# Kernel tuning notes

Measured on AMD Instinct MI355X. Metric: run time of the kernel, lower is better.

Reference implementation:

```python
import jax, jax.numpy as jnp
import numpy as np

N = 50000       # population nodes
E = 1_600_000   # edges per edge type
F_IN = 2000     # flattened individual-graph embedding (100*20)
D = 20          # hidden channels per TransformerConv head (heads=1)
NEG_SLOPE = 0.01
BN_EPS = 1e-5


def setup_inputs() -> dict:
    key = jax.random.key(0)
    ks = jax.random.split(key, 24)
    features = jax.random.normal(ks[0], (N, F_IN), jnp.float32)
    same_index = jax.random.randint(ks[1], (2, E), 0, N, dtype=jnp.int64)
    diff_index = jax.random.randint(ks[2], (2, E), 0, N, dtype=jnp.int64)
    s0 = 1.0 / np.sqrt(F_IN)
    s1 = 1.0 / np.sqrt(D)
    # layer 0 conv params, stacked over the 2 edge types (same, diff)
    W0q = jax.random.normal(ks[3], (2, F_IN, D), jnp.float32) * s0
    W0k = jax.random.normal(ks[4], (2, F_IN, D), jnp.float32) * s0
    W0v = jax.random.normal(ks[5], (2, F_IN, D), jnp.float32) * s0
    W0s = jax.random.normal(ks[6], (2, F_IN, D), jnp.float32) * s0
    b0q = jnp.zeros((2, D)); b0k = jnp.zeros((2, D))
    b0v = jnp.zeros((2, D)); b0s = jnp.zeros((2, D))
    # layers 1..3 conv params: [layer, edge_type, D, D]
    Wq = jax.random.normal(ks[7], (3, 2, D, D), jnp.float32) * s1
    Wk = jax.random.normal(ks[8], (3, 2, D, D), jnp.float32) * s1
    Wv = jax.random.normal(ks[9], (3, 2, D, D), jnp.float32) * s1
    Ws = jax.random.normal(ks[10], (3, 2, D, D), jnp.float32) * s1
    bq = jnp.zeros((3, 2, D)); bk = jnp.zeros((3, 2, D))
    bv = jnp.zeros((3, 2, D)); bs = jnp.zeros((3, 2, D))
    w1 = jnp.full((4,), 0.8, jnp.float32)
    w2 = jnp.full((4,), 0.2, jnp.float32)
    bn_gamma = jnp.ones((4, D), jnp.float32)
    bn_beta = jnp.zeros((4, D), jnp.float32)
    Wout = jax.random.normal(ks[11], (4 * D, 2), jnp.float32) / np.sqrt(4 * D)
    bout = jnp.zeros((2,), jnp.float32)
    return dict(features=features, same_index=same_index, diff_index=diff_index,
                W0q=W0q, b0q=b0q, W0k=W0k, b0k=b0k, W0v=W0v, b0v=b0v, W0s=W0s, b0s=b0s,
                Wq=Wq, bq=bq, Wk=Wk, bk=bk, Wv=Wv, bv=bv, Ws=Ws, bs=bs,
                w1=w1, w2=w2, bn_gamma=bn_gamma, bn_beta=bn_beta, Wout=Wout, bout=bout)


def _tconv(x, edge_index, Wq, bq, Wk, bk, Wv, bv, Ws, bs):
    """PyG TransformerConv, heads=1, concat=True, root_weight=True, no edge_attr."""
    src, dst = edge_index[0], edge_index[1]
    q = x @ Wq + bq   # [N, D]
    k = x @ Wk + bk
    v = x @ Wv + bv
    logits = jnp.einsum('ed,ed->e', q[dst], k[src]) / jnp.sqrt(jnp.float32(D))  # [E]
    m = jax.ops.segment_max(logits, dst, num_segments=N)
    m = jnp.where(jnp.isfinite(m), m, jnp.float32(0.0))  # nodes with no in-edges
    e = jnp.exp(logits - m[dst])
    z = jax.ops.segment_sum(e, dst, num_segments=N)
    alpha = e / (z[dst] + 1e-16)  # PyG softmax epsilon
    agg = jax.ops.segment_sum(alpha[:, None] * v[src], dst, num_segments=N)  # [N, D]
    return agg + x @ Ws + bs  # skip (root) connection


def _bn(x, gamma, beta):
    mu = x.mean(axis=0)
    var = x.var(axis=0)
    return (x - mu) * jax.lax.rsqrt(var + BN_EPS) * gamma + beta


def reference(features, same_index, diff_index,
              W0q, b0q, W0k, b0k, W0v, b0v, W0s, b0s,
              Wq, bq, Wk, bk, Wv, bv, Ws, bs,
              w1, w2, bn_gamma, bn_beta, Wout, bout):
    x = features
    fcs = []
    for l in range(4):
        if l == 0:
            p_same = (W0q[0], b0q[0], W0k[0], b0k[0], W0v[0], b0v[0], W0s[0], b0s[0])
            p_diff = (W0q[1], b0q[1], W0k[1], b0k[1], W0v[1], b0v[1], W0s[1], b0s[1])
        else:
            i = l - 1
            p_same = (Wq[i, 0], bq[i, 0], Wk[i, 0], bk[i, 0], Wv[i, 0], bv[i, 0], Ws[i, 0], bs[i, 0])
            p_diff = (Wq[i, 1], bq[i, 1], Wk[i, 1], bk[i, 1], Wv[i, 1], bv[i, 1], Ws[i, 1], bs[i, 1])
        x1 = _tconv(x, same_index, *p_same)
        x2 = _tconv(x, diff_index, *p_diff)
        t = w1[l] + w2[l]
        x = (w1[l] / t) * x1 + (w2[l] / t) * x2
        x = _bn(x, bn_gamma[l], bn_beta[l])
        x = jax.nn.leaky_relu(x, NEG_SLOPE)
        fcs.append(x)
    fc = jnp.concatenate(fcs, axis=-1)  # [N, 80]
    return fc @ Wout + bout  # [N, 2]
```

## Files before the change

### kernel.cpp

```cpp
#include <hip/hip_runtime.h>
#include <math.h>

#define N_NODES 50000
#define E_EDGES 1600000
#define F_IN    2000
#define D       20
#define NCOL    160
#define KPAD    2016
#define NBNP    64

#define INV_SQRT_D 0.22360679774997896f

typedef __bf16 bf16x8 __attribute__((ext_vector_type(8)));
typedef __bf16 bf16x4 __attribute__((ext_vector_type(4)));
typedef float  f32x4  __attribute__((ext_vector_type(4)));


__global__ void pack_kernel(
    const float* __restrict__ W0q, const float* __restrict__ W0k,
    const float* __restrict__ W0v, const float* __restrict__ W0s,
    const float* __restrict__ b0q, const float* __restrict__ b0k,
    const float* __restrict__ b0v, const float* __restrict__ b0s,
    const float* __restrict__ Wq,  const float* __restrict__ Wk,
    const float* __restrict__ Wv,  const float* __restrict__ Ws_,
    const float* __restrict__ bq,  const float* __restrict__ bk,
    const float* __restrict__ bv,  const float* __restrict__ bs_,
    __bf16* __restrict__ B0, float* __restrict__ bias0,
    float* __restrict__ WL, float* __restrict__ biasL,
    float* __restrict__ bnp, int* __restrict__ deg)
{
  long idx = (long)blockIdx.x * blockDim.x + threadIdx.x;
  if (idx < (long)NCOL*KPAD) {
    int col = (int)(idx / KPAD), k = (int)(idx % KPAD);
    int et = col / 80, r = col % 80, mat = r / 20, d = r % 20;
    const float* w = (mat==0)?W0q:(mat==1)?W0s:(mat==2)?W0k:W0v;
    float v = (k < F_IN) ? w[((size_t)et*F_IN + k)*D + d] : 0.f;
    B0[idx] = (__bf16)v;
    return;
  }
  idx -= (long)NCOL*KPAD;
  if (idx < 160) {
    int col = (int)idx;
    int et = col / 80, r = col % 80, mat = r / 20, d = r % 20;
    const float* b = (mat==0)?b0q:(mat==1)?b0s:(mat==2)?b0k:b0v;
    bias0[col] = b[et*D + d];
    return;
  }
  idx -= 160;
  if (idx < 9600) {
    int l = (int)(idx / 3200), rem = (int)(idx % 3200);
    int k = rem / NCOL, col = rem % NCOL;
    int et = col / 80, r = col % 80, mat = r / 20, d = r % 20;
    const float* w = (mat==0)?Wq:(mat==1)?Ws_:(mat==2)?Wk:Wv;
    WL[idx] = w[(((size_t)l*2 + et)*D + k)*D + d];
    return;
  }
  idx -= 9600;
  if (idx < 480) {
    int l = (int)(idx / NCOL), col = (int)(idx % NCOL);
    int et = col / 80, r = col % 80, mat = r / 20, d = r % 20;
    const float* b = (mat==0)?bq:(mat==1)?bs_:(mat==2)?bk:bv;
    biasL[idx] = b[(l*2 + et)*D + d];
    return;
  }
  idx -= 480;
  if (idx < 4*NBNP*40) { bnp[idx] = 0.f; return; }
  idx -= 4*NBNP*40;
  if (idx < 2*N_NODES) { deg[idx] = 0; return; }
}

__global__ void hist_kernel(const int* __restrict__ same, const int* __restrict__ diff,
                            int* __restrict__ deg)
{
  long i = (long)blockIdx.x * blockDim.x + threadIdx.x;
  if (i >= 2L*E_EDGES) return;
  int et = (i >= E_EDGES) ? 1 : 0;
  long e = i - (long)et*E_EDGES;
  const int* ix = et ? diff : same;
  int dst = ix[E_EDGES + e];
  atomicAdd(&deg[(size_t)et*N_NODES + dst], 1);
}

__global__ void scan_kernel(const int* __restrict__ deg,
                            int* __restrict__ rowptr0, int* __restrict__ rowptr1,
                            int* __restrict__ next0, int* __restrict__ next1)
{
  const int et = blockIdx.x;
  const int* dg = deg + (size_t)et*N_NODES;
  int* rp = et ? rowptr1 : rowptr0;
  int* np = et ? next1 : next0;
  __shared__ int part[1024];
  const int t = threadIdx.x;
  const int per = (N_NODES + 1023) / 1024;
  const int b = t * per;
  const int e = (b + per < N_NODES) ? (b + per) : N_NODES;
  int s = 0;
  for (int i = b; i < e; i++) s += dg[i];
  part[t] = s;
  __syncthreads();
  for (int o = 1; o < 1024; o <<= 1) {
    int v = (t >= o) ? part[t-o] : 0;
    __syncthreads();
    part[t] += v;
    __syncthreads();
  }
  int run = (t == 0) ? 0 : part[t-1];
  for (int i = b; i < e; i++) {
    rp[i] = run; np[i] = run;
    run += dg[i];
  }
  if (t == 0) rp[N_NODES] = part[1023];
}

#define SC_EPT 16
#define SC_CHUNK (256*SC_EPT)
__global__ void scatter_kernel(const int* __restrict__ same, const int* __restrict__ diff,
                               int* __restrict__ next0, int* __restrict__ next1,
                               int* __restrict__ adj0, int* __restrict__ adj1)
{
  const int part  = blockIdx.x & 7;
  const int chunk = blockIdx.x >> 3;
  const int lo = part * (N_NODES/8);
  const int hi = lo + (N_NODES/8);
  const long i0 = (long)chunk * SC_CHUNK + threadIdx.x;
#pragma unroll
  for (int it = 0; it < SC_EPT; ++it) {
    long i = i0 + (long)it*256;
    if (i >= 2L*E_EDGES) break;
    int et = (i >= E_EDGES) ? 1 : 0;
    long e = i - (long)et*E_EDGES;
    const int* ix = et ? diff : same;
    int dst = ix[E_EDGES + e];
    if (dst >= lo && dst < hi) {
      int src = ix[e];
      int* np  = et ? next1 : next0;
      int* adj = et ? adj1  : adj0;
      int pos = atomicAdd(&np[dst], 1);
      adj[pos] = src;
    }
  }
}

__launch_bounds__(512)
__global__ void gemm0_mfma(const float* __restrict__ A,
                           const __bf16* __restrict__ Bt,
                           const float* __restrict__ bias,
                           __bf16* __restrict__ QS,
                           __bf16* __restrict__ KV0, __bf16* __restrict__ KV1)
{
  __shared__ __bf16 as[128*32];
  const int t    = threadIdx.x;
  const int lane = t & 63;
  const int wid  = t >> 6;
  const int wr   = wid >> 1;
  const int wc   = wid & 1;
  const int rb0  = blockIdx.x * 128;

  const int srow = t >> 2;
  const int skc  = (t & 3) * 8;
  const int arow = rb0 + srow;
  const float* aptr = A + (size_t)arow * F_IN;

  const int lrow = lane & 15;
  const int lkb  = (lane >> 4) * 8;

  f32x4 acc[2][5];
#pragma unroll
  for (int i = 0; i < 2; i++)
#pragma unroll
    for (int j = 0; j < 5; j++) acc[i][j] = (f32x4){0.f,0.f,0.f,0.f};

  float4 p0, p1;
  auto loadA = [&](int k0) {
    int k = k0 + skc;
    if (arow < N_NODES) {
      if (k + 8 <= F_IN) {
        p0 = *(const float4*)(aptr + k);
        p1 = *(const float4*)(aptr + k + 4);
      } else {
        float tmp[8];
#pragma unroll
        for (int i = 0; i < 8; i++) tmp[i] = (k + i < F_IN) ? aptr[k + i] : 0.f;
        p0 = make_float4(tmp[0],tmp[1],tmp[2],tmp[3]);
        p1 = make_float4(tmp[4],tmp[5],tmp[6],tmp[7]);
      }
    } else {
      p0 = make_float4(0,0,0,0); p1 = p0;
    }
  };

  loadA(0);
  for (int s = 0; s < 63; s++) {
    bf16x8 h;
    h[0]=(__bf16)p0.x; h[1]=(__bf16)p0.y; h[2]=(__bf16)p0.z; h[3]=(__bf16)p0.w;
    h[4]=(__bf16)p1.x; h[5]=(__bf16)p1.y; h[6]=(__bf16)p1.z; h[7]=(__bf16)p1.w;
    *(bf16x8*)&as[srow*32 + skc] = h;
    __syncthreads();
    if (s + 1 < 63) loadA((s + 1) * 32);

    bf16x8 af[2];
#pragma unroll
    for (int rf = 0; rf < 2; rf++)
      af[rf] = *(bf16x8*)&as[(wr*32 + rf*16 + lrow)*32 + lkb];
    bf16x8 bfr[5];
#pragma unroll
    for (int cf = 0; cf < 5; cf++)
      bfr[cf] = *(const bf16x8*)(Bt + (size_t)(wc*80 + cf*16 + lrow)*KPAD + s*32 + lkb);
#pragma unroll
    for (int rf = 0; rf < 2; rf++)
#pragma unroll
      for (int cf = 0; cf < 5; cf++)
        acc[rf][cf] = __builtin_amdgcn_mfma_f32_16x16x32_bf16(af[rf], bfr[cf], acc[rf][cf], 0, 0, 0);
    __syncthreads();
  }

#pragma unroll
  for (int rf = 0; rf < 2; rf++) {
#pragma unroll
    for (int cf = 0; cf < 5; cf++) {
      int col = wc*80 + cf*16 + lrow;
      int et = col / 80, r = col % 80, mat = r / 20, d = r % 20;
      float bv = bias[col];
      __bf16* kvp = et ? KV1 : KV0;
#pragma unroll
      for (int j = 0; j < 4; j++) {
        int row = rb0 + wr*32 + rf*16 + (lane >> 4)*4 + j;
        if (row < N_NODES) {
          __bf16 val = (__bf16)(acc[rf][cf][j] + bv);
          if (mat < 2) QS[(size_t)row*80 + et*40 + mat*20 + d] = val;
          else         kvp[(size_t)row*64 + (mat-2)*20 + d]   = val;
        }
      }
    }
  }
}

__launch_bounds__(256)
__global__ void proj_small_kernel(const float* __restrict__ xp, const float* __restrict__ bnl,
                                  const float* __restrict__ gam, const float* __restrict__ bet,
                                  const float* __restrict__ W, const float* __restrict__ bias,
                                  __bf16* __restrict__ QS,
                                  __bf16* __restrict__ KV0, __bf16* __restrict__ KV1)
{
  __shared__ float ws[20*160];
  __shared__ float xs[16*20];
  __shared__ float Ac[20], Bc[20];
  const int t = threadIdx.x;
  const int n0 = blockIdx.x * 16;
#pragma unroll
  for (int i = 0; i < 13; i++) {
    int idx = t + i*256;
    if (idx < 3200) ws[idx] = W[idx];
  }
  if (t < 20) {
    float s1 = 0.f, s2 = 0.f;
    for (int s = 0; s < NBNP; s++) { s1 += bnl[s*40 + t]; s2 += bnl[s*40 + 20 + t]; }
    float mu  = s1 * (1.f/N_NODES);
    float var = s2 * (1.f/N_NODES) - mu*mu;
    float a = rsqrtf(var + 1e-5f) * gam[t];
    Ac[t] = a; Bc[t] = bet[t] - mu*a;
  }
  __syncthreads();
#pragma unroll
  for (int i = 0; i < 2; i++) {
    int idx = t + i*256;
    if (idx < 320) {
      int nl = idx / 20, k = idx % 20;
      int n = n0 + nl;
      float x = (n < N_NODES) ? xp[(size_t)n*D + k] : 0.f;
      float y = x*Ac[k] + Bc[k];
      xs[idx] = (y > 0.f) ? y : 0.01f*y;
    }
  }
  __syncthreads();
#pragma unroll
  for (int i = 0; i < 10; i++) {
    int idx = t + i*256;
    int nl = idx / NCOL, col = idx % NCOL;
    int n = n0 + nl;
    if (n < N_NODES) {
      float acc = bias[col];
#pragma unroll
      for (int k = 0; k < 20; k++) acc += xs[nl*20 + k] * ws[k*NCOL + col];
      int et = col / 80, r = col % 80, mat = r / 20, d = r % 20;
      __bf16 val = (__bf16)acc;
      if (mat < 2) QS[(size_t)n*80 + et*40 + mat*20 + d] = val;
      else         (et ? KV1 : KV0)[(size_t)n*64 + (mat-2)*20 + d] = val;
    }
  }
}

__launch_bounds__(256)
__global__ void attn_fused(const int* __restrict__ rp0, const int* __restrict__ adj0,
                           const int* __restrict__ rp1, const int* __restrict__ adj1,
                           const __bf16* __restrict__ QS,
                           const __bf16* __restrict__ KV0, const __bf16* __restrict__ KV1,
                           const float* __restrict__ w1, const float* __restrict__ w2, int l,
                           float* __restrict__ xpre, float* __restrict__ bnp)
{
  __shared__ float xnode[4][20];
  const int t    = threadIdx.x;
  const int wv   = t >> 6;
  const int lane = t & 63;
  const int half = lane >> 5;
  const int sl   = lane & 31;
  const int node = blockIdx.x*4 + wv;

  const int* rowptr = half ? rp1 : rp0;
  const int* adj    = half ? adj1 : adj0;
  const __bf16* kvb = half ? KV1 : KV0;
  const __bf16* rq  = QS + (size_t)node*80 + half*40;

  float qf[20];
  {
    bf16x8 q0 = *(const bf16x8*)(rq);
    bf16x8 q1 = *(const bf16x8*)(rq + 8);
    bf16x4 q2 = *(const bf16x4*)(rq + 16);
#pragma unroll
    for (int i = 0; i < 8; i++) { qf[i] = (float)q0[i]; qf[8+i] = (float)q1[i]; }
#pragma unroll
    for (int i = 0; i < 4; i++) qf[16+i] = (float)q2[i];
  }

  const int beg = rowptr[node], end = rowptr[node+1];
  float z = 0.f;
  float S[20];
#pragma unroll
  for (int d = 0; d < 20; d++) S[d] = 0.f;

  for (int i = beg + sl; i < end; i += 32) {
    const int src = adj[i];
    const __bf16* kv = kvb + (size_t)src*64;
    bf16x8 a0 = *(const bf16x8*)(kv);
    bf16x8 a1 = *(const bf16x8*)(kv + 8);
    bf16x8 a2 = *(const bf16x8*)(kv + 16);
    bf16x8 a3 = *(const bf16x8*)(kv + 24);
    bf16x8 a4 = *(const bf16x8*)(kv + 32);
    float d0 = 0.f;
#pragma unroll
    for (int j = 0; j < 8; j++) d0 += qf[j]     * (float)a0[j];
#pragma unroll
    for (int j = 0; j < 8; j++) d0 += qf[8 + j] * (float)a1[j];
#pragma unroll
    for (int j = 0; j < 4; j++) d0 += qf[16 + j]* (float)a2[j];
    const float w0 = __expf(fminf(d0*INV_SQRT_D, 80.f));
    z += w0;
#pragma unroll
    for (int d = 0; d < 4; d++) S[d]     += w0*(float)a2[4+d];
#pragma unroll
    for (int d = 0; d < 8; d++) S[4+d]   += w0*(float)a3[d];
#pragma unroll
    for (int d = 0; d < 8; d++) S[12+d]  += w0*(float)a4[d];
  }

#pragma unroll
  for (int o = 16; o >= 1; o >>= 1) {
    z += __shfl_xor(z, o, 64);
#pragma unroll
    for (int d = 0; d < 20; d++) S[d] += __shfl_xor(S[d], o, 64);
  }

  const float inv = (z > 0.f) ? 1.f/z : 0.f;
  float outv[20];
  {
    bf16x4 s0 = *(const bf16x4*)(rq + 20);
    bf16x8 s1 = *(const bf16x8*)(rq + 24);
    bf16x8 s2 = *(const bf16x8*)(rq + 32);
#pragma unroll
    for (int i = 0; i < 4; i++) outv[i] = S[i]*inv + (float)s0[i];
#pragma unroll
    for (int i = 0; i < 8; i++) { outv[4+i]  = S[4+i]*inv  + (float)s1[i];
                                  outv[12+i] = S[12+i]*inv + (float)s2[i]; }
  }

  const float wa = w1[l], wb = w2[l];
  const float c0 = wa/(wa+wb), c1 = wb/(wa+wb);
  const float cme = half ? c1 : c0;
  const float cot = half ? c0 : c1;
  float x[20];
#pragma unroll
  for (int d = 0; d < 20; d++) {
    float o2 = __shfl_xor(outv[d], 32, 64);
    x[d] = cme*outv[d] + cot*o2;
  }

  if (lane == 0) {
    float* xo = xpre + (size_t)node*D;
#pragma unroll
    for (int j = 0; j < 5; j++) {
      float4 o4 = make_float4(x[4*j], x[4*j+1], x[4*j+2], x[4*j+3]);
      *(float4*)(xo + 4*j) = o4;
    }
#pragma unroll
    for (int d = 0; d < 20; d++) xnode[wv][d] = x[d];
  }
  __syncthreads();

  if (t < 20) {
    float s1 = xnode[0][t] + xnode[1][t] + xnode[2][t] + xnode[3][t];
    float s2 = xnode[0][t]*xnode[0][t] + xnode[1][t]*xnode[1][t]
             + xnode[2][t]*xnode[2][t] + xnode[3][t]*xnode[3][t];
    float* slot = bnp + (blockIdx.x & (NBNP-1))*40;
    atomicAdd(&slot[t], s1);
    atomicAdd(&slot[20 + t], s2);
  }
}

__launch_bounds__(256)
__global__ void final_kernel(const float* __restrict__ xpre4, const float* __restrict__ bnp,
                             const float* __restrict__ gam, const float* __restrict__ bet,
                             const float* __restrict__ Wout, const float* __restrict__ bout,
                             float* __restrict__ out)
{
  __shared__ float Ac[80], Bc[80], wlds[160];
  const int t = threadIdx.x;
  if (t < 80) {
    int l = t / 20, d = t % 20;
    const float* b = bnp + l*(NBNP*40);
    float s1 = 0.f, s2 = 0.f;
    for (int s = 0; s < NBNP; s++) { s1 += b[s*40 + d]; s2 += b[s*40 + 20 + d]; }
    float mu  = s1 * (1.f/N_NODES);
    float var = s2 * (1.f/N_NODES) - mu*mu;
    float a = rsqrtf(var + 1e-5f) * gam[t];
    Ac[t] = a; Bc[t] = bet[t] - mu*a;
  }
  if (t < 160) wlds[t] = Wout[t];
  __syncthreads();

  const int n = blockIdx.x*256 + t;
  if (n >= N_NODES) return;
  float a0 = bout[0], a1 = bout[1];
#pragma unroll
  for (int l = 0; l < 4; l++) {
    const float* base = xpre4 + (size_t)l*N_NODES*D + (size_t)n*D;
#pragma unroll
    for (int d = 0; d < D; d++) {
      int idx = l*20 + d;
      float y = base[d]*Ac[idx] + Bc[idx];
      y = (y > 0.f) ? y : 0.01f*y;
      a0 += y * wlds[idx*2 + 0];
      a1 += y * wlds[idx*2 + 1];
    }
  }
  out[n*2+0] = a0;
  out[n*2+1] = a1;
}

extern "C" void kernel_launch(void* const* d_in, const int* in_sizes, int n_in,
                              void* d_out, int out_size, void* d_ws, size_t ws_size,
                              hipStream_t stream)
{
  const float* feat = (const float*)d_in[0];
  const int*   same = (const int*)d_in[1];
  const int*   diff = (const int*)d_in[2];
  const float* W0q = (const float*)d_in[3];
  const float* b0q = (const float*)d_in[4];
  const float* W0k = (const float*)d_in[5];
  const float* b0k = (const float*)d_in[6];
  const float* W0v = (const float*)d_in[7];
  const float* b0v = (const float*)d_in[8];
  const float* W0s = (const float*)d_in[9];
  const float* b0s = (const float*)d_in[10];
  const float* Wq  = (const float*)d_in[11];
  const float* bq  = (const float*)d_in[12];
  const float* Wk  = (const float*)d_in[13];
  const float* bk  = (const float*)d_in[14];
  const float* Wv  = (const float*)d_in[15];
  const float* bv  = (const float*)d_in[16];
  const float* Ws_ = (const float*)d_in[17];
  const float* bs_ = (const float*)d_in[18];
  const float* w1  = (const float*)d_in[19];
  const float* w2  = (const float*)d_in[20];
  const float* gamma = (const float*)d_in[21];
  const float* beta  = (const float*)d_in[22];
  const float* Wout  = (const float*)d_in[23];
  const float* bout  = (const float*)d_in[24];

  float* wsf  = (float*)d_ws;
  __bf16*  QS    = (__bf16*)wsf;
  __bf16*  KV0   = (__bf16*)(wsf + 2000000);
  __bf16*  KV1   = (__bf16*)(wsf + 3600000);
  float*   XPRE4 = wsf + 5200000;
  __bf16*  B0bf  = (__bf16*)(wsf + 9200000);
  float*   BIAS0 = wsf + 9361280;
  float*   WL    = wsf + 9361440;
  float*   BIASL = wsf + 9371040;
  float*   BNP   = wsf + 9371520;
  int*     ib    = (int*)(wsf + 9381760);
  int* DEG  = ib;
  int* RP0  = ib + 100000;
  int* RP1  = ib + 150004;
  int* NX0  = ib + 200008;
  int* NX1  = ib + 250008;
  int* ADJ0 = ib + 300008;
  int* ADJ1 = ib + 1900008;

  const int packN = NCOL*KPAD + 160 + 9600 + 480 + 4*NBNP*40 + 2*N_NODES;
  pack_kernel<<<(packN + 255)/256, 256, 0, stream>>>(
      W0q, W0k, W0v, W0s, b0q, b0k, b0v, b0s,
      Wq, Wk, Wv, Ws_, bq, bk, bv, bs_,
      B0bf, BIAS0, WL, BIASL, BNP, DEG);

  hist_kernel<<<(2*E_EDGES + 255)/256, 256, 0, stream>>>(same, diff, DEG);
  scan_kernel<<<2, 1024, 0, stream>>>(DEG, RP0, RP1, NX0, NX1);
  {
    const long nchunk = (2L*E_EDGES + SC_CHUNK - 1) / SC_CHUNK;
    scatter_kernel<<<(int)(nchunk*8), 256, 0, stream>>>(same, diff, NX0, NX1, ADJ0, ADJ1);
  }

  for (int l = 0; l < 4; l++) {
    if (l == 0)
      gemm0_mfma<<<(N_NODES + 127)/128, 512, 0, stream>>>(feat, B0bf, BIAS0, QS, KV0, KV1);
    else
      proj_small_kernel<<<(N_NODES + 15)/16, 256, 0, stream>>>(
          XPRE4 + (size_t)(l-1)*N_NODES*D, BNP + (l-1)*(NBNP*40),
          gamma + (l-1)*D, beta + (l-1)*D,
          WL + (size_t)(l-1)*3200, BIASL + (size_t)(l-1)*160, QS, KV0, KV1);

    attn_fused<<<N_NODES/4, 256, 0, stream>>>(
        RP0, ADJ0, RP1, ADJ1, QS, KV0, KV1, w1, w2, l,
        XPRE4 + (size_t)l*N_NODES*D, BNP + l*(NBNP*40));
  }

  final_kernel<<<(N_NODES + 255)/256, 256, 0, stream>>>(
      XPRE4, BNP, gamma, beta, Wout, bout, (float*)d_out);
}
```

Baseline: 986.9 us.

## Partition histogram by dst range, shrink gemm0 tiles, unroll attention edges, per-wave BN atomics

The degree histogram now uses the same destination-partitioned chunking as the scatter kernel, which keeps atomics localized to one eighth of the node range per block. gemm0 is launched with 64-row tiles and 256 threads instead of 128-row tiles and 512 threads. The attention loop processes two edges per lane per iteration so more gathers are in flight. BN statistics are accumulated per wave directly with atomics, dropping the shared-memory block reduction and its barrier. The risks are that the histogram now reads the edge list eight times and that there are more global atomics on the BN slots.

```diff
diff --git a/kernel.cpp b/kernel.cpp
--- a/kernel.cpp
+++ b/kernel.cpp
@@ -69,16 +69,28 @@
   if (idx < 2*N_NODES) { deg[idx] = 0; return; }
 }
 
+#define SC_EPT 16
+#define SC_CHUNK (256*SC_EPT)
+
 __global__ void hist_kernel(const int* __restrict__ same, const int* __restrict__ diff,
                             int* __restrict__ deg)
 {
-  long i = (long)blockIdx.x * blockDim.x + threadIdx.x;
-  if (i >= 2L*E_EDGES) return;
-  int et = (i >= E_EDGES) ? 1 : 0;
-  long e = i - (long)et*E_EDGES;
-  const int* ix = et ? diff : same;
-  int dst = ix[E_EDGES + e];
-  atomicAdd(&deg[(size_t)et*N_NODES + dst], 1);
+  const int part  = blockIdx.x & 7;
+  const int chunk = blockIdx.x >> 3;
+  const int lo = part * (N_NODES/8);
+  const int hi = lo + (N_NODES/8);
+  const long i0 = (long)chunk * SC_CHUNK + threadIdx.x;
+#pragma unroll
+  for (int it = 0; it < SC_EPT; ++it) {
+    long i = i0 + (long)it*256;
+    if (i >= 2L*E_EDGES) break;
+    int et = (i >= E_EDGES) ? 1 : 0;
+    long e = i - (long)et*E_EDGES;
+    const int* ix = et ? diff : same;
+    int dst = ix[E_EDGES + e];
+    if (dst >= lo && dst < hi)
+      atomicAdd(&deg[(size_t)et*N_NODES + dst], 1);
+  }
 }
 
 __global__ void scan_kernel(const int* __restrict__ deg,
@@ -112,8 +124,6 @@
   if (t == 0) rp[N_NODES] = part[1023];
 }
 
-#define SC_EPT 16
-#define SC_CHUNK (256*SC_EPT)
 __global__ void scatter_kernel(const int* __restrict__ same, const int* __restrict__ diff,
                                int* __restrict__ next0, int* __restrict__ next1,
                                int* __restrict__ adj0, int* __restrict__ adj1)
@@ -141,20 +151,20 @@
   }
 }
 
-__launch_bounds__(512)
+__launch_bounds__(256)
 __global__ void gemm0_mfma(const float* __restrict__ A,
                            const __bf16* __restrict__ Bt,
                            const float* __restrict__ bias,
                            __bf16* __restrict__ QS,
                            __bf16* __restrict__ KV0, __bf16* __restrict__ KV1)
 {
-  __shared__ __bf16 as[128*32];
+  __shared__ __bf16 as[64*32];
   const int t    = threadIdx.x;
   const int lane = t & 63;
   const int wid  = t >> 6;
   const int wr   = wid >> 1;
   const int wc   = wid & 1;
-  const int rb0  = blockIdx.x * 128;
+  const int rb0  = blockIdx.x * 64;
 
   const int srow = t >> 2;
   const int skc  = (t & 3) * 8;
@@ -298,7 +308,6 @@
                            const float* __restrict__ w1, const float* __restrict__ w2, int l,
                            float* __restrict__ xpre, float* __restrict__ bnp)
 {
-  __shared__ float xnode[4][20];
   const int t    = threadIdx.x;
   const int wv   = t >> 6;
   const int lane = t & 63;
@@ -328,14 +337,47 @@
 #pragma unroll
   for (int d = 0; d < 20; d++) S[d] = 0.f;
 
-  for (int i = beg + sl; i < end; i += 32) {
-    const int src = adj[i];
-    const __bf16* kv = kvb + (size_t)src*64;
-    bf16x8 a0 = *(const bf16x8*)(kv);
-    bf16x8 a1 = *(const bf16x8*)(kv + 8);
-    bf16x8 a2 = *(const bf16x8*)(kv + 16);
-    bf16x8 a3 = *(const bf16x8*)(kv + 24);
-    bf16x8 a4 = *(const bf16x8*)(kv + 32);
+  int i = beg + sl;
+  for (; i + 32 < end; i += 64) {
+    const int s0 = adj[i], s1 = adj[i+32];
+    const __bf16* kva = kvb + (size_t)s0*64;
+    const __bf16* kvc = kvb + (size_t)s1*64;
+    bf16x8 a0 = *(const bf16x8*)(kva);
+    bf16x8 a1 = *(const bf16x8*)(kva + 8);
+    bf16x8 a2 = *(const bf16x8*)(kva + 16);
+    bf16x8 a3 = *(const bf16x8*)(kva + 24);
+    bf16x8 a4 = *(const bf16x8*)(kva + 32);
+    bf16x8 b0 = *(const bf16x8*)(kvc);
+    bf16x8 b1 = *(const bf16x8*)(kvc + 8);
+    bf16x8 b2 = *(const bf16x8*)(kvc + 16);
+    bf16x8 b3 = *(const bf16x8*)(kvc + 24);
+    bf16x8 b4 = *(const bf16x8*)(kvc + 32);
+
+    float d0 = 0.f, d1 = 0.f;
+#pragma unroll
+    for (int j = 0; j < 8; j++) { d0 += qf[j]*(float)a0[j];     d1 += qf[j]*(float)b0[j]; }
+#pragma unroll
+    for (int j = 0; j < 8; j++) { d0 += qf[8+j]*(float)a1[j];   d1 += qf[8+j]*(float)b1[j]; }
+#pragma unroll
+    for (int j = 0; j < 4; j++) { d0 += qf[16+j]*(float)a2[j];  d1 += qf[16+j]*(float)b2[j]; }
+    const float w0 = __expf(fminf(d0*INV_SQRT_D, 80.f));
+    const float w1v= __expf(fminf(d1*INV_SQRT_D, 80.f));
+    z += w0 + w1v;
+#pragma unroll
+    for (int d = 0; d < 4; d++) S[d]     += w0*(float)a2[4+d] + w1v*(float)b2[4+d];
+#pragma unroll
+    for (int d = 0; d < 8; d++) S[4+d]   += w0*(float)a3[d]   + w1v*(float)b3[d];
+#pragma unroll
+    for (int d = 0; d < 8; d++) S[12+d]  += w0*(float)a4[d]   + w1v*(float)b4[d];
+  }
+  if (i < end) {
+    const int s0 = adj[i];
+    const __bf16* kva = kvb + (size_t)s0*64;
+    bf16x8 a0 = *(const bf16x8*)(kva);
+    bf16x8 a1 = *(const bf16x8*)(kva + 8);
+    bf16x8 a2 = *(const bf16x8*)(kva + 16);
+    bf16x8 a3 = *(const bf16x8*)(kva + 24);
+    bf16x8 a4 = *(const bf16x8*)(kva + 32);
     float d0 = 0.f;
 #pragma unroll
     for (int j = 0; j < 8; j++) d0 += qf[j]     * (float)a0[j];
@@ -367,10 +409,10 @@
     bf16x8 s1 = *(const bf16x8*)(rq + 24);
     bf16x8 s2 = *(const bf16x8*)(rq + 32);
 #pragma unroll
-    for (int i = 0; i < 4; i++) outv[i] = S[i]*inv + (float)s0[i];
-#pragma unroll
-    for (int i = 0; i < 8; i++) { outv[4+i]  = S[4+i]*inv  + (float)s1[i];
-                                  outv[12+i] = S[12+i]*inv + (float)s2[i]; }
+    for (int i2 = 0; i2 < 4; i2++) outv[i2] = S[i2]*inv + (float)s0[i2];
+#pragma unroll
+    for (int i2 = 0; i2 < 8; i2++) { outv[4+i2]  = S[4+i2]*inv  + (float)s1[i2];
+                                     outv[12+i2] = S[12+i2]*inv + (float)s2[i2]; }
   }
 
   const float wa = w1[l], wb = w2[l];
@@ -391,18 +433,15 @@
       float4 o4 = make_float4(x[4*j], x[4*j+1], x[4*j+2], x[4*j+3]);
       *(float4*)(xo + 4*j) = o4;
     }
-#pragma unroll
-    for (int d = 0; d < 20; d++) xnode[wv][d] = x[d];
-  }
-  __syncthreads();
-
-  if (t < 20) {
-    float s1 = xnode[0][t] + xnode[1][t] + xnode[2][t] + xnode[3][t];
-    float s2 = xnode[0][t]*xnode[0][t] + xnode[1][t]*xnode[1][t]
-             + xnode[2][t]*xnode[2][t] + xnode[3][t]*xnode[3][t];
-    float* slot = bnp + (blockIdx.x & (NBNP-1))*40;
-    atomicAdd(&slot[t], s1);
-    atomicAdd(&slot[20 + t], s2);
+  }
+
+  float v = x[0];
+#pragma unroll
+  for (int d = 1; d < 20; d++) v = (sl == d) ? x[d] : v;
+  if (sl < 20) {
+    float* slot = bnp + (size_t)((blockIdx.x*4 + wv) & (NBNP-1))*40;
+    if (half == 0) atomicAdd(&slot[sl], v);
+    else           atomicAdd(&slot[20 + sl], v*v);
   }
 }
 
@@ -501,16 +540,14 @@
       Wq, Wk, Wv, Ws_, bq, bk, bv, bs_,
       B0bf, BIAS0, WL, BIASL, BNP, DEG);
 
-  hist_kernel<<<(2*E_EDGES + 255)/256, 256, 0, stream>>>(same, diff, DEG);
+  const long nchunk = (2L*E_EDGES + SC_CHUNK - 1) / SC_CHUNK;
+  hist_kernel<<<(int)(nchunk*8), 256, 0, stream>>>(same, diff, DEG);
   scan_kernel<<<2, 1024, 0, stream>>>(DEG, RP0, RP1, NX0, NX1);
-  {
-    const long nchunk = (2L*E_EDGES + SC_CHUNK - 1) / SC_CHUNK;
-    scatter_kernel<<<(int)(nchunk*8), 256, 0, stream>>>(same, diff, NX0, NX1, ADJ0, ADJ1);
-  }
+  scatter_kernel<<<(int)(nchunk*8), 256, 0, stream>>>(same, diff, NX0, NX1, ADJ0, ADJ1);
 
   for (int l = 0; l < 4; l++) {
     if (l == 0)
-      gemm0_mfma<<<(N_NODES + 127)/128, 512, 0, stream>>>(feat, B0bf, BIAS0, QS, KV0, KV1);
+      gemm0_mfma<<<(N_NODES + 63)/64, 256, 0, stream>>>(feat, B0bf, BIAS0, QS, KV0, KV1);
     else
       proj_small_kernel<<<(N_NODES + 15)/16, 256, 0, stream>>>(
           XPRE4 + (size_t)(l-1)*N_NODES*D, BNP + (l-1)*(NBNP*40),
```

Result: no change. 977.1 us (-1.0%).
